# Performance work log

Measured on AMD Instinct MI355X. Metric: run time of the kernel, lower is better.

Reference implementation:

```python
import jax, jax.numpy as jnp
import numpy as np

B, L_IMG, L_TXT, DM, H, D = 1, 4096, 512, 3072, 24, 128
EPS = 1e-6


def _rms(x, scale):
    # flax nnx RMSNorm: x * rsqrt(mean(x^2) + eps) * scale
    var = jnp.mean(jnp.square(x), axis=-1, keepdims=True)
    return x * jax.lax.rsqrt(var + EPS) * scale


def _qkv(x, W, qn, kn):
    b, l = x.shape[:2]
    qkv = (x @ W).reshape(b, l, 3, H, D).transpose(2, 0, 3, 1, 4)  # [3,B,H,L,D]
    q, k, v = qkv[0], qkv[1], qkv[2]
    return _rms(q, qn), _rms(k, kn), v


def setup_inputs() -> dict:
    key = jax.random.key(0)
    ks = jax.random.split(key, 8)
    s = 0.02
    return {
        "hidden_states": jax.random.normal(ks[0], (B, L_IMG, DM), jnp.float32),
        "encoder_hidden_states": jax.random.normal(ks[1], (B, L_TXT, DM), jnp.float32),
        "image_rotary_emb": jax.random.normal(ks[2], (L_TXT + L_IMG, D // 2, 4), jnp.float32),
        "W_iqkv": jax.random.normal(ks[3], (DM, 3 * H * D), jnp.float32) * s,
        "W_eqkv": jax.random.normal(ks[4], (DM, 3 * H * D), jnp.float32) * s,
        "W_iproj": jax.random.normal(ks[5], (H * D, DM), jnp.float32) * s,
        "b_iproj": jnp.zeros((DM,), jnp.float32),
        "W_eproj": jax.random.normal(ks[6], (H * D, DM), jnp.float32) * s,
        "b_eproj": jnp.zeros((DM,), jnp.float32),
        "qn_scale": jnp.ones((D,), jnp.float32),
        "kn_scale": jnp.ones((D,), jnp.float32),
        "eqn_scale": jnp.ones((D,), jnp.float32),
        "ekn_scale": jnp.ones((D,), jnp.float32),
    }


def reference(hidden_states, encoder_hidden_states, image_rotary_emb,
              W_iqkv, W_eqkv, W_iproj, b_iproj, W_eproj, b_eproj,
              qn_scale, kn_scale, eqn_scale, ekn_scale):
    scale = D ** -0.5
    l_txt = encoder_hidden_states.shape[1]

    q, k, v = _qkv(hidden_states, W_iqkv, qn_scale, kn_scale)           # [B,H,L_img,D]
    eq, ek, ev = _qkv(encoder_hidden_states, W_eqkv, eqn_scale, ekn_scale)

    q = jnp.concatenate((eq, q), axis=2)   # [B,H,L,D], L = L_txt + L_img
    k = jnp.concatenate((ek, k), axis=2)
    v = jnp.concatenate((ev, v), axis=2)

    # RoPE: freqs_cis [L, D/2, 2, 2]
    fc = image_rotary_emb.reshape(image_rotary_emb.shape[0], image_rotary_emb.shape[1], 2, 2)

    def rope(x):
        x_ = x.reshape(*x.shape[:-1], -1, 1, 2)  # [B,H,L,D/2,1,2]
        out = fc[..., 0] * x_[..., 0] + fc[..., 1] * x_[..., 1]  # [B,H,L,D/2,2]
        return out.reshape(*x.shape).astype(x.dtype)

    q, k = rope(q), rope(k)

    # flatten heads into feature dim BEFORE attention (faithful to original)
    def merge(x):
        b, h, l, d = x.shape
        return x.transpose(0, 2, 1, 3).reshape(b, l, h * d)

    qm, km, vm = merge(q), merge(k), merge(v)  # [B,L,H*D]

    attn = jax.nn.softmax(jnp.einsum('bqd,bkd->bqk', qm, km) * scale, axis=-1)
    out = jnp.einsum('bqk,bkd->bqd', attn, vm)  # [B,L,H*D]

    ctx_out, img_out = out[:, :l_txt], out[:, l_txt:]
    img_out = img_out @ W_iproj + b_iproj
    ctx_out = ctx_out @ W_eproj + b_eproj
    return img_out, ctx_out
```

## Files before the change

kernel.cpp:

```cpp
#include <hip/hip_runtime.h>
#include <hip/hip_bf16.h>
#include <cstdint>

typedef __attribute__((ext_vector_type(8))) short u16x8;
typedef _Float16 f16_t;
typedef __attribute__((ext_vector_type(8))) f16_t f16x8;
typedef __attribute__((ext_vector_type(4))) float f32x4;

#define L_TOT 4608
#define L_TXT 512
#define L_IMG 4096
#define NH 24
#define HD 128
#define DMODEL 3072
#define NQKV 9216
#define LOG2E 1.44269504088896340736f
#define S_SHIFT 32.0f

__device__ __forceinline__ ushort f2h(float f) {
  union { f16_t h; ushort u; } c; c.h = (f16_t)f; return c.u;
}
__device__ __forceinline__ float h2f(ushort u) {
  union { ushort u; f16_t h; } c; c.u = u; return (float)c.h;
}
__device__ __forceinline__ void gload16(const ushort* g, ushort* l) {
  __builtin_amdgcn_global_load_lds((const __attribute__((address_space(1))) void*)g,
                                   (__attribute__((address_space(3))) void*)l, 16, 0, 0);
}

__global__ void cvt_f32_f16(const float* __restrict__ src, ushort* __restrict__ dst,
                            int n8) {
  const int i = blockIdx.x * 256 + threadIdx.x;
  if (i >= n8) return;
  const f32x4 a = *(const f32x4*)(src + (size_t)i * 8);
  const f32x4 b = *(const f32x4*)(src + (size_t)i * 8 + 4);
  alignas(16) ushort o[8];
#pragma unroll
  for (int j = 0; j < 4; ++j) { o[j] = f2h(a[j]); o[4 + j] = f2h(b[j]); }
  *(u16x8*)(dst + (size_t)i * 8) = *(const u16x8*)o;
}

__global__ void tconv_w(const float* __restrict__ src, int C, int c0,
                        ushort* __restrict__ dst) {
  __shared__ ushort tile[64][72];
  const int nb = blockIdx.x << 6, kb = blockIdx.y << 6;
  const int t = threadIdx.x;
  const int lr = t >> 2, lc = (t & 3) << 4;
  const float* sp = src + (size_t)(kb + lr) * C + c0 + nb + lc;
  const f32x4 v0 = *(const f32x4*)sp;
  const f32x4 v1 = *(const f32x4*)(sp + 4);
  const f32x4 v2 = *(const f32x4*)(sp + 8);
  const f32x4 v3 = *(const f32x4*)(sp + 12);
#pragma unroll
  for (int i = 0; i < 4; ++i) {
    tile[lr][lc + i]      = f2h(v0[i]);
    tile[lr][lc + 4 + i]  = f2h(v1[i]);
    tile[lr][lc + 8 + i]  = f2h(v2[i]);
    tile[lr][lc + 12 + i] = f2h(v3[i]);
  }
  __syncthreads();
  const int cl = t & 63, rb = (t >> 6) << 4;
  alignas(16) ushort o[16];
#pragma unroll
  for (int i = 0; i < 16; ++i) o[i] = tile[rb + i][cl];
  ushort* dp = dst + (size_t)(nb + cl) * DMODEL + kb + rb;
  *(u16x8*)dp       = *(const u16x8*)o;
  *(u16x8*)(dp + 8) = *(const u16x8*)(o + 8);
}

__global__ void tconv_h(const ushort* __restrict__ src, ushort* __restrict__ dst,
                        int R, int C) {
  __shared__ ushort tile[64][72];
  const int r0 = blockIdx.y << 6, c0 = blockIdx.x << 6;
  const int t = threadIdx.x;
  const int lr = t >> 2, lc = (t & 3) << 4;
  const ushort* sp = src + (size_t)(r0 + lr) * C + c0 + lc;
  const u16x8 v0 = *(const u16x8*)sp;
  const u16x8 v1 = *(const u16x8*)(sp + 8);
#pragma unroll
  for (int i = 0; i < 8; ++i) {
    tile[lr][lc + i]     = ((const ushort*)&v0)[i];
    tile[lr][lc + 8 + i] = ((const ushort*)&v1)[i];
  }
  __syncthreads();
  const int cl = t & 63, rb = (t >> 6) << 4;
  alignas(16) ushort o[16];
#pragma unroll
  for (int i = 0; i < 16; ++i) o[i] = tile[rb + i][cl];
  ushort* dp = dst + (size_t)(c0 + cl) * R + r0 + rb;
  *(u16x8*)dp       = *(const u16x8*)o;
  *(u16x8*)(dp + 8) = *(const u16x8*)(o + 8);
}

template <int MODE>
__global__ __launch_bounds__(512, 2) void gemm256(
    const ushort* __restrict__ A, int lda,
    const ushort* __restrict__ BtLo, const ushort* __restrict__ BtHi, int ldb,
    int N, int K, void* __restrict__ out0, ushort* __restrict__ out1,
    ushort* __restrict__ out2, const float* __restrict__ biasLo,
    const float* __restrict__ biasHi, int n_base) {
  __shared__ __align__(16) ushort lds[2][2][2][8192];
  int lin = blockIdx.y * gridDim.x + blockIdx.x;
  {
    const int nwg = gridDim.x * gridDim.y;
    const int q8 = nwg >> 3, r8 = nwg & 7;
    const int xcd = lin & 7, idx = lin >> 3;
    lin = (xcd < r8 ? xcd * (q8 + 1) : r8 * (q8 + 1) + (xcd - r8) * q8) + idx;
  }
  const int m0 = (lin % gridDim.x) << 8, n0 = (lin / gridDim.x) << 8;
  const ushort* Bt = (m0 < L_TXT) ? BtLo : BtHi;
  const int tid = threadIdx.x, w = tid >> 6, lane = tid & 63;
  const int wm = w >> 2, wn = w & 3;
  const int lr = lane & 15, g4 = lane >> 4;
  const int srow = lane >> 2;
  const int soff = 8 * ((lane & 3) ^ ((lane >> 3) & 3));
  f32x4 acc[8][4];
#pragma unroll
  for (int a = 0; a < 8; ++a)
#pragma unroll
    for (int b = 0; b < 4; ++b) acc[a][b] = (f32x4){0.f, 0.f, 0.f, 0.f};
  const int nt = K >> 6;

  auto stageA = [&](int h, int kt, int b) {
#pragma unroll
    for (int i = 0; i < 2; ++i) {
      const int j = w * 2 + i;
      gload16(A + (size_t)(m0 + 16 * j + srow) * lda + (kt << 6) + 32 * h + soff,
              &lds[b][h][0][j * 512]);
    }
  };
  auto stageB = [&](int h, int kt, int b) {
#pragma unroll
    for (int i = 0; i < 2; ++i) {
      const int j = w * 2 + i;
      gload16(Bt + (size_t)(n0 + 16 * j + srow) * ldb + (kt << 6) + 32 * h + soff,
              &lds[b][h][1][j * 512]);
    }
  };
  auto readA = [&](int h, int mi, int b) -> f16x8 {
    const int row = wm * 128 + mi * 16 + lr;
    const int byte = row * 64 + ((g4 ^ ((row >> 1) & 3)) << 4);
    return *(const f16x8*)((const char*)&lds[b][h][0][0] + byte);
  };
  auto readB = [&](int h, int ni, int b) -> f16x8 {
    const int row = wn * 64 + ni * 16 + lr;
    const int byte = row * 64 + ((g4 ^ ((row >> 1) & 3)) << 4);
    return *(const f16x8*)((const char*)&lds[b][h][1][0] + byte);
  };

  stageA(0, 0, 0); stageB(0, 0, 0); stageA(1, 0, 0); stageB(1, 0, 0);

  for (int kt = 0; kt < nt; ++kt) {
    const int c = kt & 1, sb = c ^ 1;
    const int st = (kt + 1 < nt) ? kt + 1 : 0;
    f16x8 bf[4], af[8];
    asm volatile("s_waitcnt vmcnt(4)" ::: "memory");
    asm volatile("s_barrier" ::: "memory");
    stageA(0, st, sb); stageB(0, st, sb);
#pragma unroll
    for (int ni = 0; ni < 4; ++ni) bf[ni] = readB(0, ni, c);
#pragma unroll
    for (int m = 0; m < 8; ++m) af[m] = readA(0, m, c);
    __builtin_amdgcn_s_setprio(1);
#pragma unroll
    for (int m = 0; m < 8; ++m)
#pragma unroll
      for (int ni = 0; ni < 4; ++ni)
        acc[m][ni] = __builtin_amdgcn_mfma_f32_16x16x32_f16(af[m], bf[ni], acc[m][ni], 0, 0, 0);
    __builtin_amdgcn_s_setprio(0);
    asm volatile("s_waitcnt vmcnt(4)" ::: "memory");
    asm volatile("s_barrier" ::: "memory");
    stageA(1, st, sb); stageB(1, st, sb);
#pragma unroll
    for (int ni = 0; ni < 4; ++ni) bf[ni] = readB(1, ni, c);
#pragma unroll
    for (int m = 0; m < 8; ++m) af[m] = readA(1, m, c);
    __builtin_amdgcn_s_setprio(1);
#pragma unroll
    for (int m = 0; m < 8; ++m)
#pragma unroll
      for (int ni = 0; ni < 4; ++ni)
        acc[m][ni] = __builtin_amdgcn_mfma_f32_16x16x32_f16(af[m], bf[ni], acc[m][ni], 0, 0, 0);
    __builtin_amdgcn_s_setprio(0);
  }

  const int rb = (lane >> 4) << 2;
  const int cl = lane & 15;
  if (MODE == 0) {
    const int g = n_base + n0;
    const int which = g / DMODEL;
    const int col0 = g - which * DMODEL;
    ushort* dst = (which == 0) ? (ushort*)out0 : (which == 1) ? out1 : out2;
#pragma unroll
    for (int mi = 0; mi < 8; ++mi)
#pragma unroll
      for (int j = 0; j < 4; ++j) {
        const int l = m0 + wm * 128 + mi * 16 + rb + j;
        const size_t rbase = (size_t)l * DMODEL + col0 + wn * 64 + cl;
#pragma unroll
        for (int ni = 0; ni < 4; ++ni) dst[rbase + ni * 16] = f2h(acc[mi][ni][j]);
      }
  } else if (MODE == 1) {
    float* outf = (float*)out0;
    const float* bias = (m0 < L_TXT) ? biasLo : biasHi;
    const int rofs = (m0 < L_TXT) ? L_IMG : -L_TXT;
    float bv[4];
#pragma unroll
    for (int ni = 0; ni < 4; ++ni) bv[ni] = bias[n0 + wn * 64 + ni * 16 + cl];
#pragma unroll
    for (int mi = 0; mi < 8; ++mi)
#pragma unroll
      for (int j = 0; j < 4; ++j) {
        const int r = m0 + wm * 128 + mi * 16 + rb + j + rofs;
        const size_t rbase = (size_t)r * N + n0 + wn * 64 + cl;
#pragma unroll
        for (int ni = 0; ni < 4; ++ni) outf[rbase + ni * 16] = acc[mi][ni][j] + bv[ni];
      }
  } else {
    ushort* outb = (ushort*)out0;
    const float sh = (MODE == 3) ? S_SHIFT : 0.0f;
#pragma unroll
    for (int mi = 0; mi < 8; ++mi)
#pragma unroll
      for (int j = 0; j < 4; ++j) {
        const int r = m0 + wm * 128 + mi * 16 + rb + j;
        const size_t rbase = (size_t)r * N + n0 + wn * 64 + cl;
#pragma unroll
        for (int ni = 0; ni < 4; ++ni) outb[rbase + ni * 16] = f2h(acc[mi][ni][j] - sh);
      }
  }
}

__global__ void norm_rope(ushort* __restrict__ Q, ushort* __restrict__ Kg,
                          const float* __restrict__ rope,
                          const float* __restrict__ qn, const float* __restrict__ kn,
                          const float* __restrict__ eqn, const float* __restrict__ ekn) {
  const int idx = (blockIdx.x << 2) + (threadIdx.x >> 6);
  const int lane = threadIdx.x & 63;
  const int h = idx % NH, l = idx / NH;
  const float* qsc = (l < L_TXT) ? eqn : qn;
  const float* ksc = (l < L_TXT) ? ekn : kn;
  const size_t base = (size_t)l * DMODEL + h * HD + (lane << 1);
  const f32x4 fcv = *(const f32x4*)(rope + ((size_t)l * 64 + lane) * 4);
  const float fa = fcv[0], fb = fcv[1], fc = fcv[2], fd = fcv[3];
  const float s0 = qsc[lane << 1], s1 = qsc[(lane << 1) + 1];
  const float t0 = ksc[lane << 1], t1 = ksc[(lane << 1) + 1];
  {
    const uint32_t qv = *(const uint32_t*)&Q[base];
    float x0 = h2f((ushort)(qv & 0xffff)), x1 = h2f((ushort)(qv >> 16));
    float ss = x0 * x0 + x1 * x1;
#pragma unroll
    for (int m = 1; m < 64; m <<= 1) ss += __shfl_xor(ss, m);
    const float r = rsqrtf(ss * (1.0f / 128.0f) + 1e-6f);
    x0 *= r * s0;
    x1 *= r * s1;
    const float o0 = (fa * x0 + fb * x1) * 0.08838834764831845f;
    const float o1 = (fc * x0 + fd * x1) * 0.08838834764831845f;
    *(uint32_t*)&Q[base] = (uint32_t)f2h(o0) | ((uint32_t)f2h(o1) << 16);
  }
  {
    const uint32_t kv = *(const uint32_t*)&Kg[base];
    float x0 = h2f((ushort)(kv & 0xffff)), x1 = h2f((ushort)(kv >> 16));
    float ss = x0 * x0 + x1 * x1;
#pragma unroll
    for (int m = 1; m < 64; m <<= 1) ss += __shfl_xor(ss, m);
    const float r = rsqrtf(ss * (1.0f / 128.0f) + 1e-6f);
    x0 *= r * t0;
    x1 *= r * t1;
    const float o0 = fa * x0 + fb * x1;
    const float o1 = fc * x0 + fd * x1;
    *(uint32_t*)&Kg[base] = (uint32_t)f2h(o0) | ((uint32_t)f2h(o1) << 16);
  }
}

__global__ void softmax_rows(ushort* __restrict__ S) {
  const int r = blockIdx.x, tid = threadIdx.x;
  ushort* Sr = S + (size_t)r * L_TOT;
  float v[18];
  float m = -3.0e38f;
#pragma unroll
  for (int j = 0; j < 18; ++j) { v[j] = h2f(Sr[tid + (j << 8)]); m = fmaxf(m, v[j]); }
#pragma unroll
  for (int o = 1; o < 64; o <<= 1) m = fmaxf(m, __shfl_xor(m, o));
  __shared__ float redm[4], reds[4];
  const int wave = tid >> 6, lane = tid & 63;
  if (lane == 0) redm[wave] = m;
  __syncthreads();
  m = fmaxf(fmaxf(redm[0], redm[1]), fmaxf(redm[2], redm[3]));
  float s = 0.f;
#pragma unroll
  for (int j = 0; j < 18; ++j) { v[j] = exp2f((v[j] - m) * LOG2E); s += v[j]; }
#pragma unroll
  for (int o = 1; o < 64; o <<= 1) s += __shfl_xor(s, o);
  if (lane == 0) reds[wave] = s;
  __syncthreads();
  const float inv = 1.0f / (reds[0] + reds[1] + reds[2] + reds[3]);
#pragma unroll
  for (int j = 0; j < 18; ++j) Sr[tid + (j << 8)] = f2h(v[j] * inv);
}

extern "C" void kernel_launch(void* const* d_in, const int* in_sizes, int n_in,
                              void* d_out, int out_size, void* d_ws, size_t ws_size,
                              hipStream_t stream) {
  (void)in_sizes; (void)n_in; (void)out_size;
  const float* hidden  = (const float*)d_in[0];
  const float* enc     = (const float*)d_in[1];
  const float* rope    = (const float*)d_in[2];
  const float* W_iqkv  = (const float*)d_in[3];
  const float* W_eqkv  = (const float*)d_in[4];
  const float* W_iproj = (const float*)d_in[5];
  const float* b_iproj = (const float*)d_in[6];
  const float* W_eproj = (const float*)d_in[7];
  const float* b_eproj = (const float*)d_in[8];
  const float* qn  = (const float*)d_in[9];
  const float* kn  = (const float*)d_in[10];
  const float* eqn = (const float*)d_in[11];
  const float* ekn = (const float*)d_in[12];
  float* out = (float*)d_out;

  const size_t SZ_S  = (size_t)L_TOT * L_TOT;
  const size_t SZ_LD = (size_t)L_TOT * DMODEL;
  const size_t SZ_WH = (size_t)L_TOT * DMODEL;
  const size_t SZ_W  = (size_t)NQKV * DMODEL;
  ushort* R0  = (ushort*)d_ws;
  ushort* CF  = R0;
  ushort* S   = R0;
  ushort* QR  = R0 + SZ_S;
  ushort* KR  = QR + SZ_LD;
  ushort* VR  = KR + SZ_LD;
  ushort* VT  = KR;
  ushort* AO  = QR;
  ushort* WTe = (ushort*)out;
  ushort* WTi = WTe + SZ_WH;
  ushort* WQe = VR + SZ_LD;
  ushort* WQi = WQe + SZ_W;
  ushort* WPi = R0;
  ushort* WPe = R0 + (size_t)DMODEL * DMODEL;
  const bool big = ws_size >= (SZ_S + 3 * SZ_LD + 2 * SZ_W) * sizeof(ushort);

  dim3 blk(256);
  cvt_f32_f16<<<dim3(L_TXT * DMODEL / 8 / 256), blk, 0, stream>>>(enc, CF,
                                                                  L_TXT * DMODEL / 8);
  cvt_f32_f16<<<dim3(L_IMG * DMODEL / 8 / 256), blk, 0, stream>>>(
      hidden, CF + (size_t)L_TXT * DMODEL, L_IMG * DMODEL / 8);
  if (big) {
    tconv_w<<<dim3(NQKV / 64, DMODEL / 64), blk, 0, stream>>>(W_eqkv, NQKV, 0, WQe);
    tconv_w<<<dim3(NQKV / 64, DMODEL / 64), blk, 0, stream>>>(W_iqkv, NQKV, 0, WQi);
    gemm256<0><<<dim3(L_TOT / 256, NQKV / 256), dim3(512), 0, stream>>>(
        CF, DMODEL, WQe, WQi, DMODEL, NQKV, DMODEL,
        QR, KR, VR, nullptr, nullptr, 0);
  } else {
    for (int h = 0; h < 2; ++h) {
      const int c0 = h * 4608;
      tconv_w<<<dim3(72, 48), blk, 0, stream>>>(W_eqkv, NQKV, c0, WTe);
      tconv_w<<<dim3(72, 48), blk, 0, stream>>>(W_iqkv, NQKV, c0, WTi);
      gemm256<0><<<dim3(L_TOT / 256, 18), dim3(512), 0, stream>>>(
          CF, DMODEL, WTe, WTi, DMODEL, 4608, DMODEL,
          QR, KR, VR, nullptr, nullptr, c0);
    }
  }
  norm_rope<<<dim3(L_TOT * NH / 4), blk, 0, stream>>>(QR, KR, rope, qn, kn, eqn, ekn);
  gemm256<3><<<dim3(L_TOT / 256, L_TOT / 256), dim3(512), 0, stream>>>(
      QR, DMODEL, KR, KR, DMODEL, L_TOT, DMODEL, S, nullptr, nullptr,
      nullptr, nullptr, 0);
  softmax_rows<<<dim3(L_TOT), blk, 0, stream>>>(S);
  tconv_h<<<dim3(48, 72), blk, 0, stream>>>(VR, VT, L_TOT, DMODEL);
  gemm256<2><<<dim3(L_TOT / 256, DMODEL / 256), dim3(512), 0, stream>>>(
      S, L_TOT, VT, VT, L_TOT, DMODEL, L_TOT, AO, nullptr, nullptr,
      nullptr, nullptr, 0);
  tconv_w<<<dim3(48, 48), blk, 0, stream>>>(W_iproj, DMODEL, 0, WPi);
  tconv_w<<<dim3(48, 48), blk, 0, stream>>>(W_eproj, DMODEL, 0, WPe);
  gemm256<1><<<dim3(L_TOT / 256, DMODEL / 256), dim3(512), 0, stream>>>(
      AO, DMODEL, WPe, WPi, DMODEL, DMODEL, DMODEL,
      out, nullptr, nullptr, b_eproj, b_iproj, 0);
}
```

Measured before the change: 820.2 us.

## Fuse exp into QK^T epilogue and defer softmax normalization to PV GEMM

Result: no change. 831.2 us (+1.4%).

```diff
diff --git a/kernel.cpp b/kernel.cpp
--- a/kernel.cpp
+++ b/kernel.cpp
@@ -22,6 +22,14 @@
 }
 __device__ __forceinline__ float h2f(ushort u) {
   union { ushort u; f16_t h; } c; c.u = u; return (float)c.h;
+}
+__device__ __forceinline__ ushort f2bf(float f) {
+  union { float f; uint32_t i; } c; c.f = f;
+  uint32_t i = c.i;
+  return (ushort)((i + 0x7FFFu + ((i >> 16) & 1u)) >> 16);
+}
+__device__ __forceinline__ float bf2f(ushort u) {
+  union { uint32_t i; float f; } c; c.i = ((uint32_t)u) << 16; return c.f;
 }
 __device__ __forceinline__ void gload16(const ushort* g, ushort* l) {
   __builtin_amdgcn_global_load_lds((const __attribute__((address_space(1))) void*)g,
@@ -68,28 +76,19 @@
   *(u16x8*)(dp + 8) = *(const u16x8*)(o + 8);
 }
 
-__global__ void tconv_h(const ushort* __restrict__ src, ushort* __restrict__ dst,
-                        int R, int C) {
-  __shared__ ushort tile[64][72];
-  const int r0 = blockIdx.y << 6, c0 = blockIdx.x << 6;
-  const int t = threadIdx.x;
-  const int lr = t >> 2, lc = (t & 3) << 4;
-  const ushort* sp = src + (size_t)(r0 + lr) * C + c0 + lc;
-  const u16x8 v0 = *(const u16x8*)sp;
-  const u16x8 v1 = *(const u16x8*)(sp + 8);
-#pragma unroll
-  for (int i = 0; i < 8; ++i) {
-    tile[lr][lc + i]     = ((const ushort*)&v0)[i];
-    tile[lr][lc + 8 + i] = ((const ushort*)&v1)[i];
-  }
+__global__ void rowsum(const ushort* __restrict__ P, float* __restrict__ RS) {
+  const int r = blockIdx.x, tid = threadIdx.x;
+  const ushort* Pr = P + (size_t)r * L_TOT;
+  float s = 0.f;
+#pragma unroll
+  for (int j = 0; j < 18; ++j) s += bf2f(Pr[tid + (j << 8)]);
+#pragma unroll
+  for (int o = 1; o < 64; o <<= 1) s += __shfl_xor(s, o);
+  __shared__ float reds[4];
+  const int wave = tid >> 6, lane = tid & 63;
+  if (lane == 0) reds[wave] = s;
   __syncthreads();
-  const int cl = t & 63, rb = (t >> 6) << 4;
-  alignas(16) ushort o[16];
-#pragma unroll
-  for (int i = 0; i < 16; ++i) o[i] = tile[rb + i][cl];
-  ushort* dp = dst + (size_t)(c0 + cl) * R + r0 + rb;
-  *(u16x8*)dp       = *(const u16x8*)o;
-  *(u16x8*)(dp + 8) = *(const u16x8*)(o + 8);
+  if (tid == 0) RS[r] = reds[0] + reds[1] + reds[2] + reds[3];
 }
 
 template <int MODE>
@@ -137,15 +136,22 @@
               &lds[b][h][1][j * 512]);
     }
   };
-  auto readA = [&](int h, int mi, int b) -> f16x8 {
+  auto readA = [&](int h, int mi, int b) -> u16x8 {
     const int row = wm * 128 + mi * 16 + lr;
     const int byte = row * 64 + ((g4 ^ ((row >> 1) & 3)) << 4);
-    return *(const f16x8*)((const char*)&lds[b][h][0][0] + byte);
-  };
-  auto readB = [&](int h, int ni, int b) -> f16x8 {
+    return *(const u16x8*)((const char*)&lds[b][h][0][0] + byte);
+  };
+  auto readB = [&](int h, int ni, int b) -> u16x8 {
     const int row = wn * 64 + ni * 16 + lr;
     const int byte = row * 64 + ((g4 ^ ((row >> 1) & 3)) << 4);
-    return *(const f16x8*)((const char*)&lds[b][h][1][0] + byte);
+    return *(const u16x8*)((const char*)&lds[b][h][1][0] + byte);
+  };
+  auto MFMA = [&](u16x8 a, u16x8 b, f32x4 c) -> f32x4 {
+    if constexpr (MODE == 2)
+      return __builtin_amdgcn_mfma_f32_16x16x32_bf16(a, b, c, 0, 0, 0);
+    else
+      return __builtin_amdgcn_mfma_f32_16x16x32_f16(
+          __builtin_bit_cast(f16x8, a), __builtin_bit_cast(f16x8, b), c, 0, 0, 0);
   };
 
   stageA(0, 0, 0); stageB(0, 0, 0); stageA(1, 0, 0); stageB(1, 0, 0);
@@ -153,7 +159,7 @@
   for (int kt = 0; kt < nt; ++kt) {
     const int c = kt & 1, sb = c ^ 1;
     const int st = (kt + 1 < nt) ? kt + 1 : 0;
-    f16x8 bf[4], af[8];
+    u16x8 bf[4], af[8];
     asm volatile("s_waitcnt vmcnt(4)" ::: "memory");
     asm volatile("s_barrier" ::: "memory");
     stageA(0, st, sb); stageB(0, st, sb);
@@ -166,7 +172,7 @@
     for (int m = 0; m < 8; ++m)
 #pragma unroll
       for (int ni = 0; ni < 4; ++ni)
-        acc[m][ni] = __builtin_amdgcn_mfma_f32_16x16x32_f16(af[m], bf[ni], acc[m][ni], 0, 0, 0);
+        acc[m][ni] = MFMA(af[m], bf[ni], acc[m][ni]);
     __builtin_amdgcn_s_setprio(0);
     asm volatile("s_waitcnt vmcnt(4)" ::: "memory");
     asm volatile("s_barrier" ::: "memory");
@@ -180,7 +186,7 @@
     for (int m = 0; m < 8; ++m)
 #pragma unroll
       for (int ni = 0; ni < 4; ++ni)
-        acc[m][ni] = __builtin_amdgcn_mfma_f32_16x16x32_f16(af[m], bf[ni], acc[m][ni], 0, 0, 0);
+        acc[m][ni] = MFMA(af[m], bf[ni], acc[m][ni]);
     __builtin_amdgcn_s_setprio(0);
   }
 
@@ -190,16 +196,42 @@
     const int g = n_base + n0;
     const int which = g / DMODEL;
     const int col0 = g - which * DMODEL;
-    ushort* dst = (which == 0) ? (ushort*)out0 : (which == 1) ? out1 : out2;
-#pragma unroll
-    for (int mi = 0; mi < 8; ++mi)
-#pragma unroll
-      for (int j = 0; j < 4; ++j) {
-        const int l = m0 + wm * 128 + mi * 16 + rb + j;
-        const size_t rbase = (size_t)l * DMODEL + col0 + wn * 64 + cl;
-#pragma unroll
-        for (int ni = 0; ni < 4; ++ni) dst[rbase + ni * 16] = f2h(acc[mi][ni][j]);
+    if (which < 2) {
+      ushort* dst = (which == 0) ? (ushort*)out0 : out1;
+#pragma unroll
+      for (int mi = 0; mi < 8; ++mi)
+#pragma unroll
+        for (int j = 0; j < 4; ++j) {
+          const int l = m0 + wm * 128 + mi * 16 + rb + j;
+          const size_t rbase = (size_t)l * DMODEL + col0 + wn * 64 + cl;
+#pragma unroll
+          for (int ni = 0; ni < 4; ++ni) dst[rbase + ni * 16] = f2h(acc[mi][ni][j]);
+        }
+    } else {
+      asm volatile("s_waitcnt vmcnt(0)" ::: "memory");
+      asm volatile("s_barrier" ::: "memory");
+      ushort* ldsT = &lds[0][0][0][0];
+#pragma unroll
+      for (int mi = 0; mi < 8; ++mi)
+#pragma unroll
+        for (int j = 0; j < 4; ++j) {
+          const int ml = wm * 128 + mi * 16 + rb + j;
+#pragma unroll
+          for (int ni = 0; ni < 4; ++ni)
+            ldsT[(wn * 64 + ni * 16 + cl) * 256 + ml] = f2bf(acc[mi][ni][j]);
+        }
+      __syncthreads();
+      const int tr = tid >> 2, tc = (tid & 3) * 64;
+#pragma unroll
+      for (int i = 0; i < 2; ++i) {
+        const int dl = i * 128 + tr;
+        ushort* dst = out2 + (size_t)(col0 + dl) * L_TOT + m0 + tc;
+        const ushort* srcL = ldsT + dl * 256 + tc;
+#pragma unroll
+        for (int v = 0; v < 8; ++v)
+          *(u16x8*)(dst + v * 8) = *(const u16x8*)(srcL + v * 8);
       }
+    }
   } else if (MODE == 1) {
     float* outf = (float*)out0;
     const float* bias = (m0 < L_TXT) ? biasLo : biasHi;
@@ -216,9 +248,20 @@
 #pragma unroll
         for (int ni = 0; ni < 4; ++ni) outf[rbase + ni * 16] = acc[mi][ni][j] + bv[ni];
       }
+  } else if (MODE == 2) {
+    ushort* outb = (ushort*)out0;
+#pragma unroll
+    for (int mi = 0; mi < 8; ++mi)
+#pragma unroll
+      for (int j = 0; j < 4; ++j) {
+        const int r = m0 + wm * 128 + mi * 16 + rb + j;
+        const float inv = 1.0f / biasLo[r];
+        const size_t rbase = (size_t)r * N + n0 + wn * 64 + cl;
+#pragma unroll
+        for (int ni = 0; ni < 4; ++ni) outb[rbase + ni * 16] = f2h(acc[mi][ni][j] * inv);
+      }
   } else {
     ushort* outb = (ushort*)out0;
-    const float sh = (MODE == 3) ? S_SHIFT : 0.0f;
 #pragma unroll
     for (int mi = 0; mi < 8; ++mi)
 #pragma unroll
@@ -226,7 +269,8 @@
         const int r = m0 + wm * 128 + mi * 16 + rb + j;
         const size_t rbase = (size_t)r * N + n0 + wn * 64 + cl;
 #pragma unroll
-        for (int ni = 0; ni < 4; ++ni) outb[rbase + ni * 16] = f2h(acc[mi][ni][j] - sh);
+        for (int ni = 0; ni < 4; ++ni)
+          outb[rbase + ni * 16] = f2bf(exp2f((acc[mi][ni][j] - S_SHIFT) * LOG2E));
       }
   }
 }
@@ -273,32 +317,6 @@
   }
 }
 
-__global__ void softmax_rows(ushort* __restrict__ S) {
-  const int r = blockIdx.x, tid = threadIdx.x;
-  ushort* Sr = S + (size_t)r * L_TOT;
-  float v[18];
-  float m = -3.0e38f;
-#pragma unroll
-  for (int j = 0; j < 18; ++j) { v[j] = h2f(Sr[tid + (j << 8)]); m = fmaxf(m, v[j]); }
-#pragma unroll
-  for (int o = 1; o < 64; o <<= 1) m = fmaxf(m, __shfl_xor(m, o));
-  __shared__ float redm[4], reds[4];
-  const int wave = tid >> 6, lane = tid & 63;
-  if (lane == 0) redm[wave] = m;
-  __syncthreads();
-  m = fmaxf(fmaxf(redm[0], redm[1]), fmaxf(redm[2], redm[3]));
-  float s = 0.f;
-#pragma unroll
-  for (int j = 0; j < 18; ++j) { v[j] = exp2f((v[j] - m) * LOG2E); s += v[j]; }
-#pragma unroll
-  for (int o = 1; o < 64; o <<= 1) s += __shfl_xor(s, o);
-  if (lane == 0) reds[wave] = s;
-  __syncthreads();
-  const float inv = 1.0f / (reds[0] + reds[1] + reds[2] + reds[3]);
-#pragma unroll
-  for (int j = 0; j < 18; ++j) Sr[tid + (j << 8)] = f2h(v[j] * inv);
-}
-
 extern "C" void kernel_launch(void* const* d_in, const int* in_sizes, int n_in,
                               void* d_out, int out_size, void* d_ws, size_t ws_size,
                               hipStream_t stream) {
@@ -328,7 +346,6 @@
   ushort* QR  = R0 + SZ_S;
   ushort* KR  = QR + SZ_LD;
   ushort* VR  = KR + SZ_LD;
-  ushort* VT  = KR;
   ushort* AO  = QR;
   ushort* WTe = (ushort*)out;
   ushort* WTi = WTe + SZ_WH;
@@ -336,6 +353,7 @@
   ushort* WQi = WQe + SZ_W;
   ushort* WPi = R0;
   ushort* WPe = R0 + (size_t)DMODEL * DMODEL;
+  float*  RS  = (float*)d_out;
   const bool big = ws_size >= (SZ_S + 3 * SZ_LD + 2 * SZ_W) * sizeof(ushort);
 
   dim3 blk(256);
@@ -363,11 +381,10 @@
   gemm256<3><<<dim3(L_TOT / 256, L_TOT / 256), dim3(512), 0, stream>>>(
       QR, DMODEL, KR, KR, DMODEL, L_TOT, DMODEL, S, nullptr, nullptr,
       nullptr, nullptr, 0);
-  softmax_rows<<<dim3(L_TOT), blk, 0, stream>>>(S);
-  tconv_h<<<dim3(48, 72), blk, 0, stream>>>(VR, VT, L_TOT, DMODEL);
+  rowsum<<<dim3(L_TOT), blk, 0, stream>>>(S, RS);
   gemm256<2><<<dim3(L_TOT / 256, DMODEL / 256), dim3(512), 0, stream>>>(
-      S, L_TOT, VT, VT, L_TOT, DMODEL, L_TOT, AO, nullptr, nullptr,
-      nullptr, nullptr, 0);
+      S, L_TOT, VR, VR, L_TOT, DMODEL, L_TOT, AO, nullptr, nullptr,
+      RS, nullptr, 0);
   tconv_w<<<dim3(48, 48), blk, 0, stream>>>(W_iproj, DMODEL, 0, WPi);
   tconv_w<<<dim3(48, 48), blk, 0, stream>>>(W_eproj, DMODEL, 0, WPe);
   gemm256<1><<<dim3(L_TOT / 256, DMODEL / 256), dim3(512), 0, stream>>>(
```
